# Optimization experiments

Measured on AMD Instinct MI355X. Metric: run time of the kernel, lower is better.

## Reference

```python
import jax, jax.numpy as jnp
import numpy as np

D_MODEL = 1024
N_HEADS = 16
DK = D_MODEL // N_HEADS


def setup_inputs() -> dict:
    key = jax.random.key(0)
    ks = jax.random.split(key, 9)
    B, T = 4, 2048
    s = 1.0 / np.sqrt(D_MODEL)
    inp = {
        "x": jax.random.normal(ks[0], (B, T, D_MODEL), dtype=jnp.float32),
        "Wq": jax.random.normal(ks[1], (D_MODEL, D_MODEL), dtype=jnp.float32) * s,
        "bq": jnp.zeros((D_MODEL,), dtype=jnp.float32),
        "Wk": jax.random.normal(ks[2], (D_MODEL, D_MODEL), dtype=jnp.float32) * s,
        "bk": jnp.zeros((D_MODEL,), dtype=jnp.float32),
        "Wv": jax.random.normal(ks[3], (D_MODEL, D_MODEL), dtype=jnp.float32) * s,
        "bv": jnp.zeros((D_MODEL,), dtype=jnp.float32),
        "Wo": jax.random.normal(ks[4], (D_MODEL, D_MODEL), dtype=jnp.float32) * s,
        "bo": jnp.zeros((D_MODEL,), dtype=jnp.float32),
    }
    return inp


def reference(x, Wq, bq, Wk, bk, Wv, bv, Wo, bo):
    B, T, D = x.shape
    H, dk = N_HEADS, DK
    scale = 1.0 / np.sqrt(dk).astype(np.float32)

    def heads(t):  # [B,T,D] -> [B,H,T,dk]
        return t.reshape(B, T, H, dk).transpose(0, 2, 1, 3)

    Q = heads(x @ Wq + bq)
    K = heads(x @ Wk + bk)
    V = heads(x @ Wv + bv)
    scores = jnp.einsum("bhqd,bhkd->bhqk", Q, K) * scale
    attn = jax.nn.softmax(scores, axis=-1)  # dropout inactive at eval
    ctx = jnp.einsum("bhqk,bhkd->bhqd", attn, V)
    ctx = ctx.transpose(0, 2, 1, 3).reshape(B, T, D)
    return ctx @ Wo + bo
```

## Files before the change

kernel.cpp:

```cpp
#include <hip/hip_runtime.h>
#include <hip/hip_bf16.h>
#include <stdint.h>

#define D_MODEL 1024
#define NHEADS  16
#define DK      64
#define TSEQ    2048
#define BATCH   4
#define MROWS   8192

typedef __attribute__((ext_vector_type(8))) short bf16x8;
typedef __attribute__((ext_vector_type(4))) float f32x4;
typedef __attribute__((ext_vector_type(16))) float f32x16;

__device__ __forceinline__ void gl_lds16(const void* g, void* l) {
  __builtin_amdgcn_global_load_lds(
      (const __attribute__((address_space(1))) unsigned int*)g,
      (__attribute__((address_space(3))) unsigned int*)l,
      16, 0, 0);
}

__device__ __forceinline__ short f2bs(float f) {
  union { __hip_bfloat16 h; short s; } u;
  u.h = __float2bfloat16(f);
  return u.s;
}

__device__ __forceinline__ uint32_t cvt_pk(float lo, float hi) {
  uint32_t r;
  asm("s_nop 1\n\tv_cvt_pk_bf16_f32 %0, %1, %2" : "=v"(r) : "v"(lo), "v"(hi));
  return r;
}

__device__ __forceinline__ void permswap(uint32_t& a, uint32_t& b) {
  asm("v_permlane32_swap_b32 %0, %1" : "+v"(a), "+v"(b));
}

__global__ void cast_x_kernel(const float* __restrict__ in, short* __restrict__ out, int n4) {
  int i = blockIdx.x * blockDim.x + threadIdx.x;
  if (i >= n4) return;
  const float4 v = reinterpret_cast<const float4*>(in)[i];
  short4 r;
  r.x = f2bs(v.x); r.y = f2bs(v.y); r.z = f2bs(v.z); r.w = f2bs(v.w);
  reinterpret_cast<short4*>(out)[i] = r;
}

__global__ void transpose_cast_kernel(const float* __restrict__ src, short* __restrict__ dst) {
  __shared__ float tile[32][33];
  const int tx = threadIdx.x, ty = threadIdx.y;
  const int n0 = blockIdx.x * 32, k0 = blockIdx.y * 32;
#pragma unroll
  for (int r = 0; r < 32; r += 8)
    tile[ty + r][tx] = src[(size_t)(k0 + ty + r) * D_MODEL + n0 + tx];
  __syncthreads();
#pragma unroll
  for (int r = 0; r < 32; r += 8)
    dst[(size_t)(n0 + ty + r) * D_MODEL + k0 + tx] = f2bs(tile[tx][ty + r]);
}

#define GEMM_MAIN_LOOP(A_, BT_)                                                     \
  __shared__ short SM[2][8192];                                                     \
  const int tid = threadIdx.x;                                                      \
  const int lane = tid & 63;                                                        \
  const int w = tid >> 6;                                                           \
  const int wm = w >> 1, wn = w & 1;                                                \
  const int rowBase = blockIdx.x * 128;                                             \
  const int colBase = blockIdx.y * 128;                                             \
  const int g = lane >> 4;                                                          \
  const int c15 = lane & 15;                                                        \
  f32x4 acc[4][4];                                                                  \
  _Pragma("unroll")                                                                 \
  for (int i = 0; i < 4; ++i)                                                       \
    _Pragma("unroll")                                                               \
    for (int j = 0; j < 4; ++j) acc[i][j] = {0.f, 0.f, 0.f, 0.f};                   \
  const int schunk = (lane & 3) ^ ((lane >> 2) & 3) ^ ((lane >> 4) & 3);            \
  const short* gA = (A_) + (size_t)(rowBase + w * 16 + (lane >> 2)) * 1024 + schunk * 8; \
  const short* gB = (BT_) + (size_t)(colBase + w * 16 + (lane >> 2)) * 1024 + schunk * 8; \
  const int ko = (g ^ (c15 & 3) ^ (c15 >> 2)) * 8;                                  \
  _Pragma("unroll")                                                                 \
  for (int c = 0; c < 2; ++c) {                                                     \
    gl_lds16(gA + (size_t)(c * 64) * 1024, &SM[0][w * 512 + c * 2048]);             \
    gl_lds16(gB + (size_t)(c * 64) * 1024, &SM[0][4096 + w * 512 + c * 2048]);      \
  }                                                                                 \
  _Pragma("unroll 2")                                                               \
  for (int kt = 0; kt < 1024; kt += 32) {                                           \
    const int buf = (kt >> 5) & 1;                                                  \
    asm volatile("s_waitcnt vmcnt(0)" ::: "memory");                                \
    __builtin_amdgcn_s_barrier();                                                   \
    __builtin_amdgcn_sched_barrier(0);                                              \
    if (kt + 32 < 1024) {                                                           \
      _Pragma("unroll")                                                             \
      for (int c = 0; c < 2; ++c) {                                                 \
        gl_lds16(gA + (size_t)(c * 64) * 1024 + kt + 32, &SM[buf ^ 1][w * 512 + c * 2048]); \
        gl_lds16(gB + (size_t)(c * 64) * 1024 + kt + 32, &SM[buf ^ 1][4096 + w * 512 + c * 2048]); \
      }                                                                             \
    }                                                                               \
    const short* smA = &SM[buf][0];                                                 \
    const short* smB = &SM[buf][4096];                                              \
    bf16x8 af[4], bfr[4];                                                           \
    _Pragma("unroll")                                                               \
    for (int i = 0; i < 4; ++i)                                                     \
      af[i] = *reinterpret_cast<const bf16x8*>(&smA[(wm * 64 + i * 16 + c15) * 32 + ko]); \
    _Pragma("unroll")                                                               \
    for (int j = 0; j < 4; ++j)                                                     \
      bfr[j] = *reinterpret_cast<const bf16x8*>(&smB[(wn * 64 + j * 16 + c15) * 32 + ko]); \
    __builtin_amdgcn_s_setprio(1);                                                  \
    _Pragma("unroll")                                                               \
    for (int i = 0; i < 4; ++i)                                                     \
      _Pragma("unroll")                                                             \
      for (int j = 0; j < 4; ++j)                                                   \
        acc[i][j] = __builtin_amdgcn_mfma_f32_16x16x32_bf16(af[i], bfr[j], acc[i][j], 0, 0, 0); \
    __builtin_amdgcn_s_setprio(0);                                                  \
  }                                                                                 \
  __syncthreads();

__global__ __launch_bounds__(256, 2) void gemm_qkv_kernel(
    const short* __restrict__ A, const short* __restrict__ BTm,
    const float* __restrict__ bq, const float* __restrict__ bk,
    const float* __restrict__ bv, short* __restrict__ Qb,
    short* __restrict__ Kb, short* __restrict__ Vtb, float CL) {
  GEMM_MAIN_LOOP(A, BTm)
  const int mat = colBase >> 10;
  if (mat == 2) {
    short* smf = &SM[0][0];
    const int d_base = wn * 64 + c15;
#pragma unroll
    for (int j = 0; j < 4; ++j) {
      const int dl = d_base + j * 16;
      const int gcol = (colBase & 1023) + dl;
      const float bb = bv[gcol];
      const int sw = (dl & 15) << 3;
#pragma unroll
      for (int i = 0; i < 4; ++i) {
        const int tb = wm * 64 + i * 16 + g * 4;
#pragma unroll
        for (int r = 0; r < 4; r += 2) {
          const uint32_t p = cvt_pk(acc[i][j][r] + bb, acc[i][j][r + 1] + bb);
          *reinterpret_cast<uint32_t*>(&smf[dl * 128 + ((tb + r) ^ sw)]) = p;
        }
      }
    }
    __syncthreads();
    const int b0 = rowBase >> 11, t0 = rowBase & 2047;
    const int vcolBase = colBase & 1023;
#pragma unroll
    for (int k = 0; k < 8; ++k) {
      const int cid = k * 256 + tid;
      const int d = cid >> 4;
      const int c = cid & 15;
      const bf16x8 vv = *reinterpret_cast<const bf16x8*>(
          &smf[d * 128 + ((c * 8) ^ ((d & 15) << 3))]);
      *reinterpret_cast<bf16x8*>(
          &Vtb[((size_t)(b0 * 1024 + vcolBase + d)) * 2048 + t0 + c * 8]) = vv;
    }
  } else {
    const float* bp = (mat == 0) ? bq : bk;
    const float scl = (mat == 0) ? CL : 1.0f;
    short* Ob = (mat == 0) ? Qb : Kb;
#pragma unroll
    for (int i = 0; i < 4; ++i) {
#pragma unroll
      for (int j = 0; j < 4; ++j) {
#pragma unroll
        for (int r = 0; r < 4; ++r) {
          const int grow = rowBase + wm * 64 + i * 16 + g * 4 + r;
          const int gcol = (colBase + wn * 64 + j * 16 + c15) & 1023;
          const float v = (acc[i][j][r] + bp[gcol]) * scl;
          const int b = grow >> 11, t = grow & 2047;
          const int h = gcol >> 6, d = gcol & 63;
          Ob[((size_t)(b * NHEADS + h) * TSEQ + t) * DK + d] = f2bs(v);
        }
      }
    }
  }
}

__global__ __launch_bounds__(256, 2) void gemm_out_kernel(
    const short* __restrict__ A, const short* __restrict__ BTm,
    const float* __restrict__ bias, float* __restrict__ Cout) {
  GEMM_MAIN_LOOP(A, BTm)
#pragma unroll
  for (int i = 0; i < 4; ++i) {
#pragma unroll
    for (int j = 0; j < 4; ++j) {
#pragma unroll
      for (int r = 0; r < 4; ++r) {
        const int grow = rowBase + wm * 64 + i * 16 + g * 4 + r;
        const int gcol = colBase + wn * 64 + j * 16 + c15;
        Cout[(size_t)grow * 1024 + gcol] = acc[i][j][r] + bias[gcol];
      }
    }
  }
}

__global__ __launch_bounds__(256, 4) void attn_kernel(
    const short* __restrict__ Qg, const short* __restrict__ Kg,
    const short* __restrict__ Vtg, short* __restrict__ ctx) {
  __shared__ short Ks[2][64 * 64];
  __shared__ short VTs[2][64 * 64];

  const int tid = threadIdx.x;
  const int lane = tid & 63;
  const int w = tid >> 6;
  const int l5 = lane >> 5;
  const int c31 = lane & 31;
  const int lid = blockIdx.x;
  const int bh = (lid >> 7) * 8 + (lid & 7);
  const int qbase = ((lid >> 3) & 15) * 128;
  const int b = bh >> 4, h = bh & 15;

  const short* Qp = Qg + (size_t)bh * TSEQ * DK;
  const short* Kp = Kg + (size_t)bh * TSEQ * DK;
  const short* Vtp = Vtg + (size_t)bh * DK * TSEQ;

  const int qrow = qbase + w * 32 + c31;

  bf16x8 qf[4];
#pragma unroll
  for (int kd = 0; kd < 4; ++kd)
    qf[kd] = *reinterpret_cast<const bf16x8*>(Qp + (size_t)qrow * DK + kd * 16 + l5 * 8);

  f32x16 o0, o1;
#pragma unroll
  for (int r = 0; r < 16; ++r) { o0[r] = 0.f; o1[r] = 0.f; }
  float l_s = 0.f;

  f32x16 z16;
#pragma unroll
  for (int r = 0; r < 16; ++r) z16[r] = 0.f;

  const int srow = w * 8 + (lane >> 3);
  const int soff = ((lane & 7) ^ (lane >> 3) ^ (w & 3)) * 8;
  const int swz = (((c31 & 7) ^ (c31 >> 3)) << 4);

  int offA[4];
#pragma unroll
  for (int kd = 0; kd < 4; ++kd)
    offA[kd] = c31 * 64 + ((((kd * 32 + l5 * 16)) ^ swz) >> 1);

#define STAGE(T, SLOT) do {                                                          \
    const int kt_ = (T) * 64;                                                        \
    _Pragma("unroll")                                                                \
    for (int c = 0; c < 2; ++c) {                                                    \
      const int row_ = c * 32 + srow;                                                \
      gl_lds16(Kp + (size_t)(kt_ + row_) * DK + soff, &Ks[SLOT][(c * 4 + w) * 512]); \
      gl_lds16(Vtp + (size_t)row_ * TSEQ + kt_ + soff, &VTs[SLOT][(c * 4 + w) * 512]); \
    }                                                                                \
  } while (0)

#define BODY(T, SLOT, PREFETCH) do {                                                 \
    asm volatile("s_waitcnt vmcnt(0)" ::: "memory");                                 \
    __builtin_amdgcn_s_barrier();                                                    \
    __builtin_amdgcn_sched_barrier(0);                                               \
    if (PREFETCH) STAGE((T) + 1, (SLOT) ^ 1);                                        \
    const short* ksb = &Ks[SLOT][0];                                                 \
    const short* vtb = &VTs[SLOT][0];                                                \
    __builtin_amdgcn_s_setprio(1);                                                   \
    const bf16x8 kf0a = *reinterpret_cast<const bf16x8*>(ksb + offA[0]);             \
    const bf16x8 kf1a = *reinterpret_cast<const bf16x8*>(ksb + 2048 + offA[0]);      \
    f32x16 s0 = __builtin_amdgcn_mfma_f32_32x32x16_bf16(kf0a, qf[0], z16, 0, 0, 0);  \
    f32x16 s1 = __builtin_amdgcn_mfma_f32_32x32x16_bf16(kf1a, qf[0], z16, 0, 0, 0);  \
    _Pragma("unroll")                                                                \
    for (int kd = 1; kd < 4; ++kd) {                                                 \
      const bf16x8 kf0 = *reinterpret_cast<const bf16x8*>(ksb + offA[kd]);           \
      const bf16x8 kf1 = *reinterpret_cast<const bf16x8*>(ksb + 2048 + offA[kd]);    \
      s0 = __builtin_amdgcn_mfma_f32_32x32x16_bf16(kf0, qf[kd], s0, 0, 0, 0);        \
      s1 = __builtin_amdgcn_mfma_f32_32x32x16_bf16(kf1, qf[kd], s1, 0, 0, 0);        \
    }                                                                                \
    __builtin_amdgcn_s_setprio(0);                                                   \
    float p0 = 0.f, p1 = 0.f, p2 = 0.f, p3 = 0.f;                                    \
    _Pragma("unroll")                                                                \
    for (int r = 0; r < 16; r += 4) {                                                \
      s0[r] = __builtin_amdgcn_exp2f(s0[r]);                                         \
      s0[r + 1] = __builtin_amdgcn_exp2f(s0[r + 1]);                                 \
      s0[r + 2] = __builtin_amdgcn_exp2f(s0[r + 2]);                                 \
      s0[r + 3] = __builtin_amdgcn_exp2f(s0[r + 3]);                                 \
      p0 += s0[r]; p1 += s0[r + 1]; p2 += s0[r + 2]; p3 += s0[r + 3];                \
    }                                                                                \
    _Pragma("unroll")                                                                \
    for (int r = 0; r < 16; r += 4) {                                                \
      s1[r] = __builtin_amdgcn_exp2f(s1[r]);                                         \
      s1[r + 1] = __builtin_amdgcn_exp2f(s1[r + 1]);                                 \
      s1[r + 2] = __builtin_amdgcn_exp2f(s1[r + 2]);                                 \
      s1[r + 3] = __builtin_amdgcn_exp2f(s1[r + 3]);                                 \
      p0 += s1[r]; p1 += s1[r + 1]; p2 += s1[r + 2]; p3 += s1[r + 3];                \
    }                                                                                \
    l_s += (p0 + p1) + (p2 + p3);                                                    \
    uint32_t wa[8], wb[8];                                                           \
    _Pragma("unroll")                                                                \
    for (int t2 = 0; t2 < 8; ++t2) {                                                 \
      wa[t2] = cvt_pk(s0[2 * t2], s0[2 * t2 + 1]);                                   \
      wb[t2] = cvt_pk(s1[2 * t2], s1[2 * t2 + 1]);                                   \
    }                                                                                \
    permswap(wa[0], wa[2]); permswap(wa[1], wa[3]);                                  \
    permswap(wa[4], wa[6]); permswap(wa[5], wa[7]);                                  \
    permswap(wb[0], wb[2]); permswap(wb[1], wb[3]);                                  \
    permswap(wb[4], wb[6]); permswap(wb[5], wb[7]);                                  \
    bf16x8 pf[4];                                                                    \
    {                                                                                \
      union { uint32_t u[4]; bf16x8 v; } fr;                                         \
      fr.u[0] = wa[0]; fr.u[1] = wa[1]; fr.u[2] = wa[2]; fr.u[3] = wa[3]; pf[0] = fr.v; \
      fr.u[0] = wa[4]; fr.u[1] = wa[5]; fr.u[2] = wa[6]; fr.u[3] = wa[7]; pf[1] = fr.v; \
      fr.u[0] = wb[0]; fr.u[1] = wb[1]; fr.u[2] = wb[2]; fr.u[3] = wb[3]; pf[2] = fr.v; \
      fr.u[0] = wb[4]; fr.u[1] = wb[5]; fr.u[2] = wb[6]; fr.u[3] = wb[7]; pf[3] = fr.v; \
    }                                                                                \
    __builtin_amdgcn_s_setprio(1);                                                   \
    _Pragma("unroll")                                                                \
    for (int ks = 0; ks < 4; ++ks) {                                                 \
      const bf16x8 vf0 = *reinterpret_cast<const bf16x8*>(vtb + offA[ks]);           \
      const bf16x8 vf1 = *reinterpret_cast<const bf16x8*>(vtb + 2048 + offA[ks]);    \
      o0 = __builtin_amdgcn_mfma_f32_32x32x16_bf16(vf0, pf[ks], o0, 0, 0, 0);        \
      o1 = __builtin_amdgcn_mfma_f32_32x32x16_bf16(vf1, pf[ks], o1, 0, 0, 0);        \
    }                                                                                \
    __builtin_amdgcn_s_setprio(0);                                                   \
  } while (0)

  STAGE(0, 0);
  for (int t = 0; t < 30; t += 2) {
    BODY(t, 0, true);
    BODY(t + 1, 1, true);
  }
  BODY(30, 0, true);
  BODY(31, 1, false);

#undef STAGE
#undef BODY

  l_s += __shfl_xor(l_s, 32, 64);

  const float inv = 1.0f / l_s;
  short* crow = ctx + ((size_t)b * TSEQ + qrow) * D_MODEL + h * 64;
#pragma unroll
  for (int r = 0; r < 16; ++r) {
    const int d = (r & 3) + 8 * (r >> 2) + 4 * l5;
    crow[d] = f2bs(o0[r] * inv);
    crow[32 + d] = f2bs(o1[r] * inv);
  }
}

extern "C" void kernel_launch(void* const* d_in, const int* in_sizes, int n_in,
                              void* d_out, int out_size, void* d_ws, size_t ws_size,
                              hipStream_t stream) {
  const float* x  = (const float*)d_in[0];
  const float* Wq = (const float*)d_in[1];
  const float* bq = (const float*)d_in[2];
  const float* Wk = (const float*)d_in[3];
  const float* bk = (const float*)d_in[4];
  const float* Wv = (const float*)d_in[5];
  const float* bv = (const float*)d_in[6];
  const float* Wo = (const float*)d_in[7];
  const float* bo = (const float*)d_in[8];
  float* out = (float*)d_out;

  short* xb   = (short*)d_ws;
  short* WqT  = xb + (size_t)MROWS * D_MODEL;
  short* WkT  = WqT + (size_t)D_MODEL * D_MODEL;
  short* WvT  = WkT + (size_t)D_MODEL * D_MODEL;
  short* WoT  = WvT + (size_t)D_MODEL * D_MODEL;
  short* Qb   = WoT + (size_t)D_MODEL * D_MODEL;
  short* Kb   = Qb + (size_t)MROWS * D_MODEL;
  short* Vtb  = Kb + (size_t)MROWS * D_MODEL;
  short* ctxb = xb;

  const float CL = 0.1803368801111204f;

  cast_x_kernel<<<(MROWS * D_MODEL / 4 + 255) / 256, 256, 0, stream>>>(x, xb, MROWS * D_MODEL / 4);
  dim3 tb(32, 8), tg(32, 32);
  transpose_cast_kernel<<<tg, tb, 0, stream>>>(Wq, WqT);
  transpose_cast_kernel<<<tg, tb, 0, stream>>>(Wk, WkT);
  transpose_cast_kernel<<<tg, tb, 0, stream>>>(Wv, WvT);
  transpose_cast_kernel<<<tg, tb, 0, stream>>>(Wo, WoT);

  gemm_qkv_kernel<<<dim3(MROWS / 128, 3 * D_MODEL / 128), 256, 0, stream>>>(
      xb, WqT, bq, bk, bv, Qb, Kb, Vtb, CL);

  attn_kernel<<<1024, 256, 0, stream>>>(Qb, Kb, Vtb, ctxb);

  gemm_out_kernel<<<dim3(MROWS / 128, D_MODEL / 128), 256, 0, stream>>>(ctxb, WoT, bo, out);
}
```

Before: 186.3 us.

## Double GEMM K-tile to 64 with new XOR swizzle; merge weight transposes into one launch

Result: faster. 167.4 us (-10.1%).

```diff
diff --git a/kernel.cpp b/kernel.cpp
--- a/kernel.cpp
+++ b/kernel.cpp
@@ -45,7 +45,14 @@
   reinterpret_cast<short4*>(out)[i] = r;
 }
 
-__global__ void transpose_cast_kernel(const float* __restrict__ src, short* __restrict__ dst) {
+__global__ void transpose_cast4_kernel(
+    const float* __restrict__ s0, const float* __restrict__ s1,
+    const float* __restrict__ s2, const float* __restrict__ s3,
+    short* __restrict__ d0, short* __restrict__ d1,
+    short* __restrict__ d2, short* __restrict__ d3) {
+  const int z = blockIdx.z;
+  const float* src = (z == 0) ? s0 : (z == 1) ? s1 : (z == 2) ? s2 : s3;
+  short* dst = (z == 0) ? d0 : (z == 1) ? d1 : (z == 2) ? d2 : d3;
   __shared__ float tile[32][33];
   const int tx = threadIdx.x, ty = threadIdx.y;
   const int n0 = blockIdx.x * 32, k0 = blockIdx.y * 32;
@@ -59,7 +66,7 @@
 }
 
 #define GEMM_MAIN_LOOP(A_, BT_)                                                     \
-  __shared__ short SM[2][8192];                                                     \
+  __shared__ short SM[2][16384];              \
   const int tid = threadIdx.x;                                                      \
   const int lane = tid & 63;                                                        \
   const int w = tid >> 6;                                                           \
@@ -73,43 +80,53 @@
   for (int i = 0; i < 4; ++i)                                                       \
     _Pragma("unroll")                                                               \
     for (int j = 0; j < 4; ++j) acc[i][j] = {0.f, 0.f, 0.f, 0.f};                   \
-  const int schunk = (lane & 3) ^ ((lane >> 2) & 3) ^ ((lane >> 4) & 3);            \
-  const short* gA = (A_) + (size_t)(rowBase + w * 16 + (lane >> 2)) * 1024 + schunk * 8; \
-  const short* gB = (BT_) + (size_t)(colBase + w * 16 + (lane >> 2)) * 1024 + schunk * 8; \
-  const int ko = (g ^ (c15 & 3) ^ (c15 >> 2)) * 8;                                  \
+  const int srow = lane >> 3;                                                       \
+  const int schunk8 = ((lane & 7) ^ srow) * 8;                                      \
+  const short* gA = (A_) + (size_t)(rowBase + w * 32 + srow) * 1024 + schunk8;      \
+  const short* gB = (BT_) + (size_t)(colBase + w * 32 + srow) * 1024 + schunk8;     \
+  const int ko0 = ((g) ^ (c15 & 7)) * 8;                                            \
+  const int ko1 = ((4 + g) ^ (c15 & 7)) * 8;                                        \
   _Pragma("unroll")                                                                 \
-  for (int c = 0; c < 2; ++c) {                                                     \
-    gl_lds16(gA + (size_t)(c * 64) * 1024, &SM[0][w * 512 + c * 2048]);             \
-    gl_lds16(gB + (size_t)(c * 64) * 1024, &SM[0][4096 + w * 512 + c * 2048]);      \
+  for (int c = 0; c < 4; ++c) {                                                     \
+    gl_lds16(gA + (size_t)(c * 8) * 1024, &SM[0][(w * 32 + c * 8) * 64]);           \
+    gl_lds16(gB + (size_t)(c * 8) * 1024, &SM[0][8192 + (w * 32 + c * 8) * 64]);    \
   }                                                                                 \
   _Pragma("unroll 2")                                                               \
-  for (int kt = 0; kt < 1024; kt += 32) {                                           \
-    const int buf = (kt >> 5) & 1;                                                  \
+  for (int kt = 0; kt < 1024; kt += 64) {                                           \
+    const int buf = (kt >> 6) & 1;                                                  \
     asm volatile("s_waitcnt vmcnt(0)" ::: "memory");                                \
     __builtin_amdgcn_s_barrier();                                                   \
     __builtin_amdgcn_sched_barrier(0);                                              \
-    if (kt + 32 < 1024) {                                                           \
+    if (kt + 64 < 1024) {                                                           \
       _Pragma("unroll")                                                             \
-      for (int c = 0; c < 2; ++c) {                                                 \
-        gl_lds16(gA + (size_t)(c * 64) * 1024 + kt + 32, &SM[buf ^ 1][w * 512 + c * 2048]); \
-        gl_lds16(gB + (size_t)(c * 64) * 1024 + kt + 32, &SM[buf ^ 1][4096 + w * 512 + c * 2048]); \
+      for (int c = 0; c < 4; ++c) {                                                 \
+        gl_lds16(gA + (size_t)(c * 8) * 1024 + kt + 64, &SM[buf ^ 1][(w * 32 + c * 8) * 64]); \
+        gl_lds16(gB + (size_t)(c * 8) * 1024 + kt + 64, &SM[buf ^ 1][8192 + (w * 32 + c * 8) * 64]); \
       }                                                                             \
     }                                                                               \
     const short* smA = &SM[buf][0];                                                 \
-    const short* smB = &SM[buf][4096];                                              \
-    bf16x8 af[4], bfr[4];                                                           \
+    const short* smB = &SM[buf][8192];                                              \
+    bf16x8 af[4][2], bfr[4][2];                                                     \
     _Pragma("unroll")                                                               \
-    for (int i = 0; i < 4; ++i)                                                     \
-      af[i] = *reinterpret_cast<const bf16x8*>(&smA[(wm * 64 + i * 16 + c15) * 32 + ko]); \
+    for (int i = 0; i < 4; ++i) {                                                   \
+      const int rb = (wm * 64 + i * 16 + c15) * 64;                                 \
+      af[i][0] = *reinterpret_cast<const bf16x8*>(&smA[rb + ko0]);                  \
+      af[i][1] = *reinterpret_cast<const bf16x8*>(&smA[rb + ko1]);                  \
+    }                                                                               \
     _Pragma("unroll")                                                               \
-    for (int j = 0; j < 4; ++j)                                                     \
-      bfr[j] = *reinterpret_cast<const bf16x8*>(&smB[(wn * 64 + j * 16 + c15) * 32 + ko]); \
+    for (int j = 0; j < 4; ++j) {                                                   \
+      const int rb = (wn * 64 + j * 16 + c15) * 64;                                 \
+      bfr[j][0] = *reinterpret_cast<const bf16x8*>(&smB[rb + ko0]);                 \
+      bfr[j][1] = *reinterpret_cast<const bf16x8*>(&smB[rb + ko1]);                 \
+    }                                                                               \
     __builtin_amdgcn_s_setprio(1);                                                  \
     _Pragma("unroll")                                                               \
-    for (int i = 0; i < 4; ++i)                                                     \
+    for (int kk = 0; kk < 2; ++kk)                                                  \
       _Pragma("unroll")                                                             \
-      for (int j = 0; j < 4; ++j)                                                   \
-        acc[i][j] = __builtin_amdgcn_mfma_f32_16x16x32_bf16(af[i], bfr[j], acc[i][j], 0, 0, 0); \
+      for (int i = 0; i < 4; ++i)                                                   \
+        _Pragma("unroll")                                                           \
+        for (int j = 0; j < 4; ++j)                                                 \
+          acc[i][j] = __builtin_amdgcn_mfma_f32_16x16x32_bf16(af[i][kk], bfr[j][kk], acc[i][j], 0, 0, 0); \
     __builtin_amdgcn_s_setprio(0);                                                  \
   }                                                                                 \
   __syncthreads();
@@ -365,11 +382,8 @@
   const float CL = 0.1803368801111204f;
 
   cast_x_kernel<<<(MROWS * D_MODEL / 4 + 255) / 256, 256, 0, stream>>>(x, xb, MROWS * D_MODEL / 4);
-  dim3 tb(32, 8), tg(32, 32);
-  transpose_cast_kernel<<<tg, tb, 0, stream>>>(Wq, WqT);
-  transpose_cast_kernel<<<tg, tb, 0, stream>>>(Wk, WkT);
-  transpose_cast_kernel<<<tg, tb, 0, stream>>>(Wv, WvT);
-  transpose_cast_kernel<<<tg, tb, 0, stream>>>(Wo, WoT);
+  transpose_cast4_kernel<<<dim3(32, 32, 4), dim3(32, 8), 0, stream>>>(
+      Wq, Wk, Wv, Wo, WqT, WkT, WvT, WoT);
 
   gemm_qkv_kernel<<<dim3(MROWS / 128, 3 * D_MODEL / 128), 256, 0, stream>>>(
       xb, WqT, bq, bk, bv, Qb, Kb, Vtb, CL);
```
